# Kernel tuning notes

Hardware: AMD Instinct MI355X
Metric: run time of the kernel (lower is better)

Reference implementation:

```python
import jax, jax.numpy as jnp
import numpy as np

B, C, H, W = 8, 512, 32, 32
NUM_HEADS, D_K = 8, 64
EPS = 1e-5


def setup_inputs() -> dict:
    key = jax.random.key(0)
    ks = jax.random.split(key, 6)
    s = 1.0 / np.sqrt(C)
    return {
        "x": jax.random.normal(ks[0], (B, C, H, W), dtype=jnp.float32),
        "wq": jax.random.uniform(ks[1], (C, NUM_HEADS * D_K), jnp.float32, -s, s),
        "bq": jnp.zeros((NUM_HEADS * D_K,), jnp.float32),
        "wk": jax.random.uniform(ks[2], (C, NUM_HEADS * D_K), jnp.float32, -s, s),
        "bk": jnp.zeros((NUM_HEADS * D_K,), jnp.float32),
        "wv": jax.random.uniform(ks[3], (C, NUM_HEADS * D_K), jnp.float32, -s, s),
        "bv": jnp.zeros((NUM_HEADS * D_K,), jnp.float32),
        "ln_g": jnp.ones((C,), jnp.float32),
        "ln_b": jnp.zeros((C,), jnp.float32),
        "wo": jax.random.uniform(ks[4], (NUM_HEADS * D_K, C), jnp.float32, -s, s),
        "bo": jnp.zeros((C,), jnp.float32),
    }


def reference(x, wq, bq, wk, bk, wv, bv, ln_g, ln_b, wo, bo):
    b, c, h, w = x.shape
    seq = h * w
    # [B, C, H, W] -> [B, S, C]
    t = x.reshape(b, c, seq).transpose(0, 2, 1)
    residual = t
    # LayerNorm over channel dim
    mu = jnp.mean(t, axis=-1, keepdims=True)
    var = jnp.var(t, axis=-1, keepdims=True)
    tn = (t - mu) * jax.lax.rsqrt(var + EPS) * ln_g + ln_b
    # QKV projections -> [B, S, h, d]
    q = (tn @ wq + bq).reshape(b, seq, NUM_HEADS, D_K)
    k = (tn @ wk + bk).reshape(b, seq, NUM_HEADS, D_K)
    v = (tn @ wv + bv).reshape(b, seq, NUM_HEADS, D_K)
    scores = jnp.einsum("bqhd,bkhd->bhqk", q, k) / np.sqrt(D_K).astype(np.float32)
    attn = jax.nn.softmax(scores, axis=-1)
    out = jnp.einsum("bhqk,bkhd->bqhd", attn, v).reshape(b, seq, NUM_HEADS * D_K)
    out = out @ wo + bo
    return out + residual
```

## Files before the change

kernel.cpp:

```cpp
#include <hip/hip_runtime.h>
#include <hip/hip_bf16.h>
#include <stdint.h>

#define BB 8
#define CC 512
#define SS 1024
#define NH 8
#define DK 64
#define MM (BB*SS)
#define PQ 72
#define LNP 40

typedef __attribute__((ext_vector_type(8))) short bf16x8;
typedef __attribute__((ext_vector_type(4))) float f32x4;

__device__ inline float b2f(unsigned short u) {
    union { unsigned int i; float f; } x; x.i = ((unsigned int)u) << 16; return x.f;
}
__device__ inline unsigned short f2b(float f) {
    union { float f; unsigned int i; } x; x.f = f;
    unsigned int r = (x.i + 0x7FFFu + ((x.i >> 16) & 1u)) >> 16;
    return (unsigned short)r;
}
__device__ inline unsigned int cvtpk(float lo, float hi) {
    unsigned int r;
    asm("v_cvt_pk_bf16_f32 %0, %1, %2" : "=v"(r) : "v"(lo), "v"(hi));
    return r;
}
__device__ inline f32x4 mfma16(bf16x8 a, bf16x8 b, f32x4 c) {
    return __builtin_amdgcn_mfma_f32_16x16x32_bf16(a, b, c, 0, 0, 0);
}
__device__ __forceinline__ void gload16(const void* g, void* l) {
    __builtin_amdgcn_global_load_lds(
        (const __attribute__((address_space(1))) void*)g,
        (__attribute__((address_space(3))) void*)l, 16, 0, 0);
}

__global__ void __launch_bounds__(256) wtrans_kernel(const float* __restrict__ wq,
                                                     const float* __restrict__ wk,
                                                     const float* __restrict__ wv,
                                                     const float* __restrict__ wo,
                                                     unsigned short* __restrict__ wT) {
    __shared__ float lds[64][65];
    const float* w = (blockIdx.z == 0) ? wq : (blockIdx.z == 1) ? wk : (blockIdx.z == 2) ? wv : wo;
    unsigned short* o = wT + (size_t)blockIdx.z * (512 * 512);
    const int n0 = blockIdx.x * 64, k0 = blockIdx.y * 64;
    const int t = threadIdx.x;
    {
        const int nl = (t & 15) * 4, kr = t >> 4;
#pragma unroll
        for (int i = 0; i < 4; ++i) {
            float4 v = *(const float4*)(w + (size_t)(k0 + kr + i * 16) * 512 + n0 + nl);
            lds[kr + i * 16][nl] = v.x; lds[kr + i * 16][nl + 1] = v.y;
            lds[kr + i * 16][nl + 2] = v.z; lds[kr + i * 16][nl + 3] = v.w;
        }
    }
    __syncthreads();
    {
        const int k8 = (t & 7) * 8, nr = t >> 3;
#pragma unroll
        for (int ii = 0; ii < 2; ++ii) {
            int n = nr + ii * 32;
            unsigned short pk[8];
#pragma unroll
            for (int e = 0; e < 8; ++e) pk[e] = f2b(lds[k8 + e][n]);
            *(uint4*)&o[(size_t)(n0 + n) * 512 + k0 + k8] = *(uint4*)pk;
        }
    }
}

__global__ void __launch_bounds__(256) xlnf_kernel(const float* __restrict__ x,
                                                   const float* __restrict__ g,
                                                   const float* __restrict__ bta,
                                                   unsigned short* __restrict__ xt,
                                                   unsigned short* __restrict__ tn) {
    __shared__ unsigned short raw[512 * LNP];
    __shared__ float2 red[32][33];
    __shared__ float2 stf[32];
    const int b = blockIdx.y, s0 = blockIdx.x * 32;
    const int t = threadIdx.x;
    const int sl4 = (t & 7) * 4, crow = t >> 3;
    float sum[4] = {0.f, 0.f, 0.f, 0.f}, sq[4] = {0.f, 0.f, 0.f, 0.f};
#pragma unroll
    for (int ci = 0; ci < 16; ++ci) {
        const int c = crow + 32 * ci;
        float4 v = *(const float4*)(x + ((size_t)b * 512 + c) * 1024 + s0 + sl4);
        sum[0] += v.x; sq[0] += v.x * v.x;
        sum[1] += v.y; sq[1] += v.y * v.y;
        sum[2] += v.z; sq[2] += v.z * v.z;
        sum[3] += v.w; sq[3] += v.w * v.w;
        const int swz = ((c >> 6) & 3) << 3;
        uint2 pk;
        pk.x = (unsigned int)f2b(v.x) | ((unsigned int)f2b(v.y) << 16);
        pk.y = (unsigned int)f2b(v.z) | ((unsigned int)f2b(v.w) << 16);
        *(uint2*)&raw[c * LNP + (sl4 ^ swz)] = pk;
    }
#pragma unroll
    for (int e = 0; e < 4; ++e) red[crow][sl4 + e] = make_float2(sum[e], sq[e]);
    __syncthreads();
    if (t < 32) {
        float s = 0.f, q = 0.f;
#pragma unroll
        for (int cg = 0; cg < 32; ++cg) { s += red[cg][t].x; q += red[cg][t].y; }
        float mean = s * (1.f / 512.f);
        float var = q * (1.f / 512.f) - mean * mean;
        stf[t] = make_float2(mean, rsqrtf(var + 1e-5f));
    }
    __syncthreads();
    {
        const int srow = t >> 3, cb = (t & 7) * 64;
        const float2 st = stf[srow];
        const size_t orow = ((size_t)b * 1024 + s0 + srow) * 512;
#pragma unroll
        for (int cc = 0; cc < 64; cc += 8) {
            const int c0 = cb + cc;
            unsigned short rv[8], nv[8];
            const float4 g0 = *(const float4*)(g + c0), g1 = *(const float4*)(g + c0 + 4);
            const float4 b0 = *(const float4*)(bta + c0), b1 = *(const float4*)(bta + c0 + 4);
            const float gg[8] = {g0.x, g0.y, g0.z, g0.w, g1.x, g1.y, g1.z, g1.w};
            const float bb[8] = {b0.x, b0.y, b0.z, b0.w, b1.x, b1.y, b1.z, b1.w};
#pragma unroll
            for (int e = 0; e < 8; ++e) {
                const int c = c0 + e;
                const int swz = ((c >> 6) & 3) << 3;
                unsigned short u = raw[c * LNP + (srow ^ swz)];
                rv[e] = u;
                nv[e] = f2b((b2f(u) - st.x) * st.y * gg[e] + bb[e]);
            }
            *(uint4*)&xt[orow + c0] = *(uint4*)rv;
            *(uint4*)&tn[orow + c0] = *(uint4*)nv;
        }
    }
}

template <bool SWAP>
__device__ inline void gemm_tile(const unsigned short* __restrict__ A,
                                 const unsigned short* __restrict__ Bt,
                                 int m0, int n0,
                                 unsigned short (*A_lds)[128 * 64],
                                 unsigned short (*B_lds)[128 * 64],
                                 f32x4 acc[4][4]) {
    const int t = threadIdx.x;
    const int lane = t & 63, w = t >> 6;
    const int l15 = lane & 15, l4 = lane >> 4;
    const int wm = (w >> 1) * 64, wn = (w & 1) * 64;
    auto STAGE = [&](int bi, int kt) {
#pragma unroll
        for (int i = 0; i < 4; ++i) {
            int chunk = i * 256 + t;
            int row = chunk >> 3, kc = (chunk & 7) * 8;
            gload16(A + (size_t)(m0 + row) * 512 + kt * 64 + kc, &A_lds[bi][chunk * 8]);
            gload16(Bt + (size_t)(n0 + row) * 512 + kt * 64 + kc, &B_lds[bi][chunk * 8]);
        }
    };
    STAGE(0, 0);
    __syncthreads();
#pragma unroll 1
    for (int kt = 0; kt < 8; ++kt) {
        const int bi = kt & 1;
        if (kt < 7) STAGE(bi ^ 1, kt + 1);
#pragma unroll
        for (int kk = 0; kk < 2; ++kk) {
            bf16x8 af[4], bfr[4];
#pragma unroll
            for (int i = 0; i < 4; ++i)
                af[i] = *(const bf16x8*)&A_lds[bi][(wm + i * 16 + l15) * 64 + kk * 32 + l4 * 8];
#pragma unroll
            for (int j = 0; j < 4; ++j)
                bfr[j] = *(const bf16x8*)&B_lds[bi][(wn + j * 16 + l15) * 64 + kk * 32 + l4 * 8];
#pragma unroll
            for (int i = 0; i < 4; ++i)
#pragma unroll
                for (int j = 0; j < 4; ++j)
                    acc[i][j] = SWAP ? mfma16(bfr[j], af[i], acc[i][j])
                                     : mfma16(af[i], bfr[j], acc[i][j]);
        }
        __syncthreads();
    }
}

__global__ void __launch_bounds__(256) gemm_qkv_kernel(const unsigned short* __restrict__ tn,
                                                       const unsigned short* __restrict__ wT,
                                                       const float* __restrict__ bq,
                                                       const float* __restrict__ bk,
                                                       const float* __restrict__ bv,
                                                       unsigned short* __restrict__ outbase) {
    __shared__ alignas(16) unsigned short A_lds[2][128 * 64];
    __shared__ alignas(16) unsigned short B_lds[2][128 * 64];
    const int z = blockIdx.z;
    const unsigned short* Bt = wT + (size_t)z * (512 * 512);
    const float* bias = (z == 0) ? bq : (z == 1) ? bk : bv;
    const int m0 = blockIdx.x * 128, n0 = blockIdx.y * 128;
    f32x4 acc[4][4];
    const f32x4 z4 = {0.f, 0.f, 0.f, 0.f};
#pragma unroll
    for (int i = 0; i < 4; ++i)
#pragma unroll
        for (int j = 0; j < 4; ++j) acc[i][j] = z4;
    const int lane = threadIdx.x & 63, w = threadIdx.x >> 6;
    const int l15 = lane & 15, l4 = lane >> 4;
    const int wm = (w >> 1) * 64, wn = (w & 1) * 64;
    if (z < 2) {
        gemm_tile<true>(tn, Bt, m0, n0, A_lds, B_lds, acc);
        unsigned short* out = outbase + (size_t)z * MM * 512;
        float4 bias4[4];
#pragma unroll
        for (int j = 0; j < 4; ++j)
            bias4[j] = *(const float4*)(bias + n0 + wn + j * 16 + l4 * 4);
#pragma unroll
        for (int i = 0; i < 4; ++i) {
            const size_t row = (size_t)(m0 + wm + i * 16 + l15);
#pragma unroll
            for (int j = 0; j < 4; ++j) {
                const int nc = n0 + wn + j * 16 + l4 * 4;
                uint2 pk;
                pk.x = (unsigned int)f2b(acc[i][j][0] + bias4[j].x) |
                       ((unsigned int)f2b(acc[i][j][1] + bias4[j].y) << 16);
                pk.y = (unsigned int)f2b(acc[i][j][2] + bias4[j].z) |
                       ((unsigned int)f2b(acc[i][j][3] + bias4[j].w) << 16);
                *(uint2*)&out[row * 512 + nc] = pk;
            }
        }
    } else {
        gemm_tile<false>(tn, Bt, m0, n0, A_lds, B_lds, acc);
        unsigned short* vt = outbase + (size_t)2 * MM * 512;
#pragma unroll
        for (int i = 0; i < 4; ++i)
#pragma unroll
            for (int j = 0; j < 4; ++j) {
                int col = n0 + wn + j * 16 + l15;
                float bcol = bias[col];
                int rowb = m0 + wm + i * 16 + l4 * 4;
                int bi = rowb >> 10, s0 = rowb & 1023;
                uint2 pk;
                pk.x = (unsigned int)f2b(acc[i][j][0] + bcol) |
                       ((unsigned int)f2b(acc[i][j][1] + bcol) << 16);
                pk.y = (unsigned int)f2b(acc[i][j][2] + bcol) |
                       ((unsigned int)f2b(acc[i][j][3] + bcol) << 16);
                *(uint2*)&vt[((size_t)bi * 512 + col) * 1024 + s0] = pk;
            }
    }
}

__global__ void __launch_bounds__(512) attn_kernel(const unsigned short* __restrict__ q,
                                                   const unsigned short* __restrict__ k,
                                                   const unsigned short* __restrict__ vt,
                                                   unsigned short* __restrict__ o) {
    __shared__ alignas(16) unsigned short Kl[2][64 * 64];
    __shared__ alignas(16) unsigned short Vl[2][64 * 64];
    __shared__ alignas(16) unsigned short Pl[8][16 * PQ];
    const int pid = blockIdx.x;
    const int g = (pid >> 6) * 8 + (pid & 7);
    const int qt = (pid >> 3) & 7;
    const int b = g >> 3, h = g & 7;
    const int t = threadIdx.x, lane = t & 63, w = t >> 6;
    const int l15 = lane & 15, l4 = lane >> 4;

    const float QSC = 0.125f * 1.44269504f;
    const int qrow = qt * 128 + w * 16 + l15;
    const unsigned short* qp = q + ((size_t)(b * SS + qrow)) * 512 + h * 64;
    bf16x8 qf[2];
#pragma unroll
    for (int kk = 0; kk < 2; ++kk) {
        bf16x8 tmp = *(const bf16x8*)(qp + kk * 32 + l4 * 8);
#pragma unroll
        for (int e = 0; e < 8; ++e)
            tmp[e] = (short)f2b(b2f((unsigned short)tmp[e]) * QSC);
        qf[kk] = tmp;
    }

    const int srow = t >> 3;
    const int scb = ((t & 7) * 16) ^ ((srow & 7) << 4);
    const char* kptr = (const char*)(k + ((size_t)(b * SS) + srow) * 512 + h * 64) + scb;
    const char* vptr = (const char*)(vt + ((size_t)(b * NH + h) * DK + srow) * SS) + scb;

    float m_run = -1e30f, l_run = 0.f;
    f32x4 acc_o[4];
    const f32x4 z4 = {0.f, 0.f, 0.f, 0.f};
#pragma unroll
    for (int j = 0; j < 4; ++j) acc_o[j] = z4;

    gload16(kptr, &Kl[0][t * 8]);
    gload16(vptr, &Vl[0][t * 8]);
    kptr += 64 * 512 * 2;
    vptr += 64 * 2;
    __syncthreads();

#pragma unroll 1
    for (int kt = 0; kt < 16; ++kt) {
        const int bi = kt & 1;
        if (kt < 15) {
            gload16(kptr, &Kl[bi ^ 1][t * 8]);
            gload16(vptr, &Vl[bi ^ 1][t * 8]);
            kptr += 64 * 512 * 2;
            vptr += 64 * 2;
        }

        f32x4 sc[4];
#pragma unroll
        for (int j = 0; j < 4; ++j) sc[j] = z4;
#pragma unroll
        for (int kk = 0; kk < 2; ++kk)
#pragma unroll
            for (int j = 0; j < 4; ++j) {
                int row = j * 16 + l15;
                int cb = (kk * 64 + l4 * 16) ^ ((row & 7) << 4);
                bf16x8 kf = *(const bf16x8*)((const char*)Kl[bi] + row * 128 + cb);
                sc[j] = mfma16(kf, qf[kk], sc[j]);
            }

        float mx = fmaxf(fmaxf(sc[0][0], sc[0][1]), fmaxf(sc[0][2], sc[0][3]));
#pragma unroll
        for (int j = 1; j < 4; ++j)
            mx = fmaxf(mx, fmaxf(fmaxf(sc[j][0], sc[j][1]), fmaxf(sc[j][2], sc[j][3])));
        mx = fmaxf(mx, __shfl_xor(mx, 16));
        mx = fmaxf(mx, __shfl_xor(mx, 32));
        const float mnew = fmaxf(m_run, mx);
        const float scl = exp2f(m_run - mnew);
        m_run = mnew;

        float p[4][4], lsum = 0.f;
#pragma unroll
        for (int j = 0; j < 4; ++j)
#pragma unroll
            for (int r = 0; r < 4; ++r) {
                p[j][r] = exp2f(sc[j][r] - mnew);
                lsum += p[j][r];
            }
        l_run = l_run * scl + lsum;

#pragma unroll
        for (int j = 0; j < 4; ++j) {
            uint2 pk;
            pk.x = cvtpk(p[j][0], p[j][1]);
            pk.y = cvtpk(p[j][2], p[j][3]);
            *(uint2*)&Pl[w][l15 * PQ + j * 16 + l4 * 4] = pk;
        }

        float scl_r[4];
#pragma unroll
        for (int r = 0; r < 4; ++r) scl_r[r] = __shfl(scl, (l4 << 2) | r);
#pragma unroll
        for (int j = 0; j < 4; ++j)
#pragma unroll
            for (int r = 0; r < 4; ++r) acc_o[j][r] *= scl_r[r];

#pragma unroll
        for (int kk = 0; kk < 2; ++kk) {
            bf16x8 pf = *(const bf16x8*)&Pl[w][l15 * PQ + kk * 32 + l4 * 8];
#pragma unroll
            for (int j = 0; j < 4; ++j) {
                int row = j * 16 + l15;
                int cb = (kk * 64 + l4 * 16) ^ ((row & 7) << 4);
                bf16x8 vf = *(const bf16x8*)((const char*)Vl[bi] + row * 128 + cb);
                acc_o[j] = mfma16(pf, vf, acc_o[j]);
            }
        }

        __syncthreads();
    }

    float l_tot = l_run;
    l_tot += __shfl_xor(l_tot, 16);
    l_tot += __shfl_xor(l_tot, 32);
    float l_r[4];
#pragma unroll
    for (int r = 0; r < 4; ++r) l_r[r] = __shfl(l_tot, (l4 << 2) | r);

#pragma unroll
    for (int j = 0; j < 4; ++j)
#pragma unroll
        for (int r = 0; r < 4; ++r) {
            int row = qt * 128 + w * 16 + l4 * 4 + r;
            float val = acc_o[j][r] / l_r[r];
            o[((size_t)(b * SS + row)) * 512 + h * 64 + j * 16 + l15] = f2b(val);
        }
}

__global__ void __launch_bounds__(256) gemm_out_kernel(const unsigned short* __restrict__ ao,
                                                       const unsigned short* __restrict__ woT,
                                                       const float* __restrict__ bo,
                                                       const unsigned short* __restrict__ xt,
                                                       float* __restrict__ out) {
    __shared__ alignas(16) unsigned short A_lds[2][128 * 64];
    __shared__ alignas(16) unsigned short B_lds[2][128 * 64];
    const int m0 = blockIdx.x * 128, n0 = blockIdx.y * 128;
    f32x4 acc[4][4];
    const f32x4 z4 = {0.f, 0.f, 0.f, 0.f};
#pragma unroll
    for (int i = 0; i < 4; ++i)
#pragma unroll
        for (int j = 0; j < 4; ++j) acc[i][j] = z4;
    gemm_tile<true>(ao, woT, m0, n0, A_lds, B_lds, acc);
    const int lane = threadIdx.x & 63, w = threadIdx.x >> 6;
    const int l15 = lane & 15, l4 = lane >> 4;
    const int wm = (w >> 1) * 64, wn = (w & 1) * 64;
    float4 bias4[4];
#pragma unroll
    for (int j = 0; j < 4; ++j)
        bias4[j] = *(const float4*)(bo + n0 + wn + j * 16 + l4 * 4);
#pragma unroll
    for (int i = 0; i < 4; ++i) {
        const size_t row = (size_t)(m0 + wm + i * 16 + l15);
#pragma unroll
        for (int j = 0; j < 4; ++j) {
            const int nc = n0 + wn + j * 16 + l4 * 4;
            uint2 rv = *(const uint2*)&xt[row * 512 + nc];
            float4 o4;
            o4.x = acc[i][j][0] + bias4[j].x + b2f((unsigned short)(rv.x & 0xffff));
            o4.y = acc[i][j][1] + bias4[j].y + b2f((unsigned short)(rv.x >> 16));
            o4.z = acc[i][j][2] + bias4[j].z + b2f((unsigned short)(rv.y & 0xffff));
            o4.w = acc[i][j][3] + bias4[j].w + b2f((unsigned short)(rv.y >> 16));
            *(float4*)&out[row * 512 + nc] = o4;
        }
    }
}

extern "C" void kernel_launch(void* const* d_in, const int* in_sizes, int n_in,
                              void* d_out, int out_size, void* d_ws, size_t ws_size,
                              hipStream_t stream) {
    const float* x   = (const float*)d_in[0];
    const float* wq  = (const float*)d_in[1];
    const float* bq  = (const float*)d_in[2];
    const float* wk  = (const float*)d_in[3];
    const float* bk  = (const float*)d_in[4];
    const float* wv  = (const float*)d_in[5];
    const float* bv  = (const float*)d_in[6];
    const float* lng = (const float*)d_in[7];
    const float* lnb = (const float*)d_in[8];
    const float* wo  = (const float*)d_in[9];
    const float* bo  = (const float*)d_in[10];
    float* out = (float*)d_out;

    unsigned short* ws  = (unsigned short*)d_ws;
    const size_t M1 = (size_t)1024 * 1024;
    unsigned short* tn   = ws;
    unsigned short* qkvb = ws + 4 * M1;
    unsigned short* wT   = ws + 16 * M1;
    unsigned short* xt   = ws + 17 * M1;
    unsigned short* ao   = tn;

    wtrans_kernel<<<dim3(8, 8, 4), 256, 0, stream>>>(wq, wk, wv, wo, wT);
    xlnf_kernel<<<dim3(32, 8), 256, 0, stream>>>(x, lng, lnb, xt, tn);
    gemm_qkv_kernel<<<dim3(64, 4, 3), 256, 0, stream>>>(tn, wT, bq, bk, bv, qkvb);
    attn_kernel<<<512, 512, 0, stream>>>(qkvb,
                                         qkvb + (size_t)MM * 512,
                                         qkvb + (size_t)2 * MM * 512,
                                         ao);
    gemm_out_kernel<<<dim3(64, 4), 256, 0, stream>>>(ao, wT + (size_t)3 * 512 * 512, bo, xt, out);
}
```

Measured before the change: 181.4 us.

## Merge prep kernels, fuse QKV GEMMs sharing A tile, swizzle LDS layout

Combines the weight transpose and the LayerNorm kernels into one launch that dispatches on block index. Rewrites the QKV GEMM so each block loads one 128-row A tile and computes Q, K and V for a 64-column slice, so the activation tile is reused across three weights instead of being loaded three times. Adds an XOR swizzle to the LDS layout of the GEMM tiles to reduce bank conflicts on fragment reads. The trade-off is fewer blocks per GEMM launch, higher register pressure from 24 accumulators, and larger shared memory in the prep kernel.

```diff
diff --git a/kernel.cpp b/kernel.cpp
--- a/kernel.cpp
+++ b/kernel.cpp
@@ -36,99 +36,102 @@
         (__attribute__((address_space(3))) void*)l, 16, 0, 0);
 }
 
-__global__ void __launch_bounds__(256) wtrans_kernel(const float* __restrict__ wq,
-                                                     const float* __restrict__ wk,
-                                                     const float* __restrict__ wv,
-                                                     const float* __restrict__ wo,
-                                                     unsigned short* __restrict__ wT) {
-    __shared__ float lds[64][65];
-    const float* w = (blockIdx.z == 0) ? wq : (blockIdx.z == 1) ? wk : (blockIdx.z == 2) ? wv : wo;
-    unsigned short* o = wT + (size_t)blockIdx.z * (512 * 512);
-    const int n0 = blockIdx.x * 64, k0 = blockIdx.y * 64;
-    const int t = threadIdx.x;
-    {
-        const int nl = (t & 15) * 4, kr = t >> 4;
-#pragma unroll
-        for (int i = 0; i < 4; ++i) {
-            float4 v = *(const float4*)(w + (size_t)(k0 + kr + i * 16) * 512 + n0 + nl);
-            lds[kr + i * 16][nl] = v.x; lds[kr + i * 16][nl + 1] = v.y;
-            lds[kr + i * 16][nl + 2] = v.z; lds[kr + i * 16][nl + 3] = v.w;
-        }
-    }
-    __syncthreads();
-    {
-        const int k8 = (t & 7) * 8, nr = t >> 3;
-#pragma unroll
-        for (int ii = 0; ii < 2; ++ii) {
-            int n = nr + ii * 32;
-            unsigned short pk[8];
-#pragma unroll
-            for (int e = 0; e < 8; ++e) pk[e] = f2b(lds[k8 + e][n]);
-            *(uint4*)&o[(size_t)(n0 + n) * 512 + k0 + k8] = *(uint4*)pk;
-        }
-    }
-}
-
-__global__ void __launch_bounds__(256) xlnf_kernel(const float* __restrict__ x,
+__global__ void __launch_bounds__(256) prep_kernel(const float* __restrict__ wq,
+                                                   const float* __restrict__ wk,
+                                                   const float* __restrict__ wv,
+                                                   const float* __restrict__ wo,
+                                                   unsigned short* __restrict__ wT,
+                                                   const float* __restrict__ x,
                                                    const float* __restrict__ g,
                                                    const float* __restrict__ bta,
                                                    unsigned short* __restrict__ xt,
                                                    unsigned short* __restrict__ tn) {
-    __shared__ unsigned short raw[512 * LNP];
-    __shared__ float2 red[32][33];
-    __shared__ float2 stf[32];
-    const int b = blockIdx.y, s0 = blockIdx.x * 32;
+    __shared__ alignas(16) char smem[49664];
     const int t = threadIdx.x;
-    const int sl4 = (t & 7) * 4, crow = t >> 3;
-    float sum[4] = {0.f, 0.f, 0.f, 0.f}, sq[4] = {0.f, 0.f, 0.f, 0.f};
-#pragma unroll
-    for (int ci = 0; ci < 16; ++ci) {
-        const int c = crow + 32 * ci;
-        float4 v = *(const float4*)(x + ((size_t)b * 512 + c) * 1024 + s0 + sl4);
-        sum[0] += v.x; sq[0] += v.x * v.x;
-        sum[1] += v.y; sq[1] += v.y * v.y;
-        sum[2] += v.z; sq[2] += v.z * v.z;
-        sum[3] += v.w; sq[3] += v.w * v.w;
-        const int swz = ((c >> 6) & 3) << 3;
-        uint2 pk;
-        pk.x = (unsigned int)f2b(v.x) | ((unsigned int)f2b(v.y) << 16);
-        pk.y = (unsigned int)f2b(v.z) | ((unsigned int)f2b(v.w) << 16);
-        *(uint2*)&raw[c * LNP + (sl4 ^ swz)] = pk;
-    }
-#pragma unroll
-    for (int e = 0; e < 4; ++e) red[crow][sl4 + e] = make_float2(sum[e], sq[e]);
-    __syncthreads();
-    if (t < 32) {
-        float s = 0.f, q = 0.f;
-#pragma unroll
-        for (int cg = 0; cg < 32; ++cg) { s += red[cg][t].x; q += red[cg][t].y; }
-        float mean = s * (1.f / 512.f);
-        float var = q * (1.f / 512.f) - mean * mean;
-        stf[t] = make_float2(mean, rsqrtf(var + 1e-5f));
-    }
-    __syncthreads();
-    {
-        const int srow = t >> 3, cb = (t & 7) * 64;
-        const float2 st = stf[srow];
-        const size_t orow = ((size_t)b * 1024 + s0 + srow) * 512;
-#pragma unroll
-        for (int cc = 0; cc < 64; cc += 8) {
-            const int c0 = cb + cc;
-            unsigned short rv[8], nv[8];
-            const float4 g0 = *(const float4*)(g + c0), g1 = *(const float4*)(g + c0 + 4);
-            const float4 b0 = *(const float4*)(bta + c0), b1 = *(const float4*)(bta + c0 + 4);
-            const float gg[8] = {g0.x, g0.y, g0.z, g0.w, g1.x, g1.y, g1.z, g1.w};
-            const float bb[8] = {b0.x, b0.y, b0.z, b0.w, b1.x, b1.y, b1.z, b1.w};
-#pragma unroll
-            for (int e = 0; e < 8; ++e) {
-                const int c = c0 + e;
-                const int swz = ((c >> 6) & 3) << 3;
-                unsigned short u = raw[c * LNP + (srow ^ swz)];
-                rv[e] = u;
-                nv[e] = f2b((b2f(u) - st.x) * st.y * gg[e] + bb[e]);
-            }
-            *(uint4*)&xt[orow + c0] = *(uint4*)rv;
-            *(uint4*)&tn[orow + c0] = *(uint4*)nv;
+    if (blockIdx.x < 256) {
+        float (*lds)[65] = (float(*)[65])smem;
+        const int bz = blockIdx.x >> 6, bx = (blockIdx.x >> 3) & 7, by = blockIdx.x & 7;
+        const float* w = (bz == 0) ? wq : (bz == 1) ? wk : (bz == 2) ? wv : wo;
+        unsigned short* o = wT + (size_t)bz * (512 * 512);
+        const int n0 = bx * 64, k0 = by * 64;
+        {
+            const int nl = (t & 15) * 4, kr = t >> 4;
+#pragma unroll
+            for (int i = 0; i < 4; ++i) {
+                float4 v = *(const float4*)(w + (size_t)(k0 + kr + i * 16) * 512 + n0 + nl);
+                lds[kr + i * 16][nl] = v.x; lds[kr + i * 16][nl + 1] = v.y;
+                lds[kr + i * 16][nl + 2] = v.z; lds[kr + i * 16][nl + 3] = v.w;
+            }
+        }
+        __syncthreads();
+        {
+            const int k8 = (t & 7) * 8, nr = t >> 3;
+#pragma unroll
+            for (int ii = 0; ii < 2; ++ii) {
+                int n = nr + ii * 32;
+                unsigned short pk[8];
+#pragma unroll
+                for (int e = 0; e < 8; ++e) pk[e] = f2b(lds[k8 + e][n]);
+                *(uint4*)&o[(size_t)(n0 + n) * 512 + k0 + k8] = *(uint4*)pk;
+            }
+        }
+    } else {
+        unsigned short* raw = (unsigned short*)smem;
+        float2 (*red)[33] = (float2(*)[33])(smem + 40960);
+        float2* stf = (float2*)(smem + 49408);
+        const int idx = blockIdx.x - 256;
+        const int b = idx >> 5, s0 = (idx & 31) * 32;
+        const int sl4 = (t & 7) * 4, crow = t >> 3;
+        float sum[4] = {0.f, 0.f, 0.f, 0.f}, sq[4] = {0.f, 0.f, 0.f, 0.f};
+#pragma unroll
+        for (int ci = 0; ci < 16; ++ci) {
+            const int c = crow + 32 * ci;
+            float4 v = *(const float4*)(x + ((size_t)b * 512 + c) * 1024 + s0 + sl4);
+            sum[0] += v.x; sq[0] += v.x * v.x;
+            sum[1] += v.y; sq[1] += v.y * v.y;
+            sum[2] += v.z; sq[2] += v.z * v.z;
+            sum[3] += v.w; sq[3] += v.w * v.w;
+            const int swz = ((c >> 6) & 3) << 3;
+            uint2 pk;
+            pk.x = (unsigned int)f2b(v.x) | ((unsigned int)f2b(v.y) << 16);
+            pk.y = (unsigned int)f2b(v.z) | ((unsigned int)f2b(v.w) << 16);
+            *(uint2*)&raw[c * LNP + (sl4 ^ swz)] = pk;
+        }
+#pragma unroll
+        for (int e = 0; e < 4; ++e) red[crow][sl4 + e] = make_float2(sum[e], sq[e]);
+        __syncthreads();
+        if (t < 32) {
+            float s = 0.f, q = 0.f;
+#pragma unroll
+            for (int cg = 0; cg < 32; ++cg) { s += red[cg][t].x; q += red[cg][t].y; }
+            float mean = s * (1.f / 512.f);
+            float var = q * (1.f / 512.f) - mean * mean;
+            stf[t] = make_float2(mean, rsqrtf(var + 1e-5f));
+        }
+        __syncthreads();
+        {
+            const int srow = t >> 3, cb = (t & 7) * 64;
+            const float2 st = stf[srow];
+            const size_t orow = ((size_t)b * 1024 + s0 + srow) * 512;
+#pragma unroll
+            for (int cc = 0; cc < 64; cc += 8) {
+                const int c0 = cb + cc;
+                unsigned short rv[8], nv[8];
+                const float4 g0 = *(const float4*)(g + c0), g1 = *(const float4*)(g + c0 + 4);
+                const float4 b0 = *(const float4*)(bta + c0), b1 = *(const float4*)(bta + c0 + 4);
+                const float gg[8] = {g0.x, g0.y, g0.z, g0.w, g1.x, g1.y, g1.z, g1.w};
+                const float bb[8] = {b0.x, b0.y, b0.z, b0.w, b1.x, b1.y, b1.z, b1.w};
+#pragma unroll
+                for (int e = 0; e < 8; ++e) {
+                    const int c = c0 + e;
+                    const int swz = ((c >> 6) & 3) << 3;
+                    unsigned short u = raw[c * LNP + (srow ^ swz)];
+                    rv[e] = u;
+                    nv[e] = f2b((b2f(u) - st.x) * st.y * gg[e] + bb[e]);
+                }
+                *(uint4*)&xt[orow + c0] = *(uint4*)rv;
+                *(uint4*)&tn[orow + c0] = *(uint4*)nv;
+            }
         }
     }
 }
@@ -148,9 +151,12 @@
 #pragma unroll
         for (int i = 0; i < 4; ++i) {
             int chunk = i * 256 + t;
-            int row = chunk >> 3, kc = (chunk & 7) * 8;
-            gload16(A + (size_t)(m0 + row) * 512 + kt * 64 + kc, &A_lds[bi][chunk * 8]);
-            gload16(Bt + (size_t)(n0 + row) * 512 + kt * 64 + kc, &B_lds[bi][chunk * 8]);
+            int row = chunk >> 3;
+            int sb = ((chunk & 7) * 16) ^ ((row & 7) << 4);
+            gload16((const char*)(A + (size_t)(m0 + row) * 512 + kt * 64) + sb,
+                    &A_lds[bi][chunk * 8]);
+            gload16((const char*)(Bt + (size_t)(n0 + row) * 512 + kt * 64) + sb,
+                    &B_lds[bi][chunk * 8]);
         }
     };
     STAGE(0, 0);
@@ -163,11 +169,17 @@
         for (int kk = 0; kk < 2; ++kk) {
             bf16x8 af[4], bfr[4];
 #pragma unroll
-            for (int i = 0; i < 4; ++i)
-                af[i] = *(const bf16x8*)&A_lds[bi][(wm + i * 16 + l15) * 64 + kk * 32 + l4 * 8];
-#pragma unroll
-            for (int j = 0; j < 4; ++j)
-                bfr[j] = *(const bf16x8*)&B_lds[bi][(wn + j * 16 + l15) * 64 + kk * 32 + l4 * 8];
+            for (int i = 0; i < 4; ++i) {
+                int row = wm + i * 16 + l15;
+                int cb = (kk * 64 + l4 * 16) ^ ((row & 7) << 4);
+                af[i] = *(const bf16x8*)((const char*)A_lds[bi] + row * 128 + cb);
+            }
+#pragma unroll
+            for (int j = 0; j < 4; ++j) {
+                int row = wn + j * 16 + l15;
+                int cb = (kk * 64 + l4 * 16) ^ ((row & 7) << 4);
+                bfr[j] = *(const bf16x8*)((const char*)B_lds[bi] + row * 128 + cb);
+            }
 #pragma unroll
             for (int i = 0; i < 4; ++i)
 #pragma unroll
@@ -179,65 +191,121 @@
     }
 }
 
-__global__ void __launch_bounds__(256) gemm_qkv_kernel(const unsigned short* __restrict__ tn,
-                                                       const unsigned short* __restrict__ wT,
-                                                       const float* __restrict__ bq,
-                                                       const float* __restrict__ bk,
-                                                       const float* __restrict__ bv,
-                                                       unsigned short* __restrict__ outbase) {
+__global__ void __launch_bounds__(256) gemm_qkvf_kernel(const unsigned short* __restrict__ tn,
+                                                        const unsigned short* __restrict__ wT,
+                                                        const float* __restrict__ bq,
+                                                        const float* __restrict__ bk,
+                                                        const float* __restrict__ bv,
+                                                        unsigned short* __restrict__ outbase) {
     __shared__ alignas(16) unsigned short A_lds[2][128 * 64];
-    __shared__ alignas(16) unsigned short B_lds[2][128 * 64];
-    const int z = blockIdx.z;
-    const unsigned short* Bt = wT + (size_t)z * (512 * 512);
-    const float* bias = (z == 0) ? bq : (z == 1) ? bk : bv;
-    const int m0 = blockIdx.x * 128, n0 = blockIdx.y * 128;
-    f32x4 acc[4][4];
+    __shared__ alignas(16) unsigned short B_lds[2][3][64 * 64];
+    const int m0 = blockIdx.x * 128, n0 = blockIdx.y * 64;
+    const int t = threadIdx.x, lane = t & 63, w = t >> 6;
+    const int l15 = lane & 15, l4 = lane >> 4;
+    const int wm = w * 32;
+    f32x4 acc[3][2][4];
     const f32x4 z4 = {0.f, 0.f, 0.f, 0.f};
 #pragma unroll
-    for (int i = 0; i < 4; ++i)
-#pragma unroll
-        for (int j = 0; j < 4; ++j) acc[i][j] = z4;
-    const int lane = threadIdx.x & 63, w = threadIdx.x >> 6;
-    const int l15 = lane & 15, l4 = lane >> 4;
-    const int wm = (w >> 1) * 64, wn = (w & 1) * 64;
-    if (z < 2) {
-        gemm_tile<true>(tn, Bt, m0, n0, A_lds, B_lds, acc);
+    for (int z = 0; z < 3; ++z)
+#pragma unroll
+        for (int i = 0; i < 2; ++i)
+#pragma unroll
+            for (int j = 0; j < 4; ++j) acc[z][i][j] = z4;
+
+    auto STAGE = [&](int bi, int kt) {
+#pragma unroll
+        for (int i = 0; i < 4; ++i) {
+            int chunk = i * 256 + t;
+            int row = chunk >> 3;
+            int sb = ((chunk & 7) * 16) ^ ((row & 7) << 4);
+            gload16((const char*)(tn + (size_t)(m0 + row) * 512 + kt * 64) + sb,
+                    &A_lds[bi][chunk * 8]);
+        }
+#pragma unroll
+        for (int z = 0; z < 3; ++z)
+#pragma unroll
+            for (int i = 0; i < 2; ++i) {
+                int chunk = i * 256 + t;
+                int row = chunk >> 3;
+                int sb = ((chunk & 7) * 16) ^ ((row & 7) << 4);
+                gload16((const char*)(wT + (size_t)z * 512 * 512 +
+                                      (size_t)(n0 + row) * 512 + kt * 64) + sb,
+                        &B_lds[bi][z][chunk * 8]);
+            }
+    };
+    STAGE(0, 0);
+    __syncthreads();
+#pragma unroll 1
+    for (int kt = 0; kt < 8; ++kt) {
+        const int bi = kt & 1;
+        if (kt < 7) STAGE(bi ^ 1, kt + 1);
+#pragma unroll
+        for (int kk = 0; kk < 2; ++kk) {
+            bf16x8 af[2];
+#pragma unroll
+            for (int i = 0; i < 2; ++i) {
+                int row = wm + i * 16 + l15;
+                int cb = (kk * 64 + l4 * 16) ^ ((row & 7) << 4);
+                af[i] = *(const bf16x8*)((const char*)A_lds[bi] + row * 128 + cb);
+            }
+#pragma unroll
+            for (int z = 0; z < 3; ++z) {
+                bf16x8 bfr[4];
+#pragma unroll
+                for (int j = 0; j < 4; ++j) {
+                    int row = j * 16 + l15;
+                    int cb = (kk * 64 + l4 * 16) ^ ((row & 7) << 4);
+                    bfr[j] = *(const bf16x8*)((const char*)B_lds[bi][z] + row * 128 + cb);
+                }
+#pragma unroll
+                for (int i = 0; i < 2; ++i)
+#pragma unroll
+                    for (int j = 0; j < 4; ++j)
+                        acc[z][i][j] = (z < 2) ? mfma16(bfr[j], af[i], acc[z][i][j])
+                                               : mfma16(af[i], bfr[j], acc[z][i][j]);
+            }
+        }
+        __syncthreads();
+    }
+#pragma unroll
+    for (int z = 0; z < 2; ++z) {
+        const float* bias = (z == 0) ? bq : bk;
         unsigned short* out = outbase + (size_t)z * MM * 512;
         float4 bias4[4];
 #pragma unroll
         for (int j = 0; j < 4; ++j)
-            bias4[j] = *(const float4*)(bias + n0 + wn + j * 16 + l4 * 4);
-#pragma unroll
-        for (int i = 0; i < 4; ++i) {
+            bias4[j] = *(const float4*)(bias + n0 + j * 16 + l4 * 4);
+#pragma unroll
+        for (int i = 0; i < 2; ++i) {
             const size_t row = (size_t)(m0 + wm + i * 16 + l15);
 #pragma unroll
             for (int j = 0; j < 4; ++j) {
-                const int nc = n0 + wn + j * 16 + l4 * 4;
+                const int nc = n0 + j * 16 + l4 * 4;
                 uint2 pk;
-                pk.x = (unsigned int)f2b(acc[i][j][0] + bias4[j].x) |
-                       ((unsigned int)f2b(acc[i][j][1] + bias4[j].y) << 16);
-                pk.y = (unsigned int)f2b(acc[i][j][2] + bias4[j].z) |
-                       ((unsigned int)f2b(acc[i][j][3] + bias4[j].w) << 16);
+                pk.x = (unsigned int)f2b(acc[z][i][j][0] + bias4[j].x) |
+                       ((unsigned int)f2b(acc[z][i][j][1] + bias4[j].y) << 16);
+                pk.y = (unsigned int)f2b(acc[z][i][j][2] + bias4[j].z) |
+                       ((unsigned int)f2b(acc[z][i][j][3] + bias4[j].w) << 16);
                 *(uint2*)&out[row * 512 + nc] = pk;
             }
         }
-    } else {
-        gemm_tile<false>(tn, Bt, m0, n0, A_lds, B_lds, acc);
+    }
+    {
         unsigned short* vt = outbase + (size_t)2 * MM * 512;
 #pragma unroll
-        for (int i = 0; i < 4; ++i)
+        for (int i = 0; i < 2; ++i)
 #pragma unroll
             for (int j = 0; j < 4; ++j) {
-                int col = n0 + wn + j * 16 + l15;
-                float bcol = bias[col];
+                int col = n0 + j * 16 + l15;
+                float bcol = bv[col];
                 int rowb = m0 + wm + i * 16 + l4 * 4;
-                int bi = rowb >> 10, s0 = rowb & 1023;
+                int bi_ = rowb >> 10, s0 = rowb & 1023;
                 uint2 pk;
-                pk.x = (unsigned int)f2b(acc[i][j][0] + bcol) |
-                       ((unsigned int)f2b(acc[i][j][1] + bcol) << 16);
-                pk.y = (unsigned int)f2b(acc[i][j][2] + bcol) |
-                       ((unsigned int)f2b(acc[i][j][3] + bcol) << 16);
-                *(uint2*)&vt[((size_t)bi * 512 + col) * 1024 + s0] = pk;
+                pk.x = (unsigned int)f2b(acc[2][i][j][0] + bcol) |
+                       ((unsigned int)f2b(acc[2][i][j][1] + bcol) << 16);
+                pk.y = (unsigned int)f2b(acc[2][i][j][2] + bcol) |
+                       ((unsigned int)f2b(acc[2][i][j][3] + bcol) << 16);
+                *(uint2*)&vt[((size_t)bi_ * 512 + col) * 1024 + s0] = pk;
             }
     }
 }
@@ -440,9 +508,8 @@
     unsigned short* xt   = ws + 17 * M1;
     unsigned short* ao   = tn;
 
-    wtrans_kernel<<<dim3(8, 8, 4), 256, 0, stream>>>(wq, wk, wv, wo, wT);
-    xlnf_kernel<<<dim3(32, 8), 256, 0, stream>>>(x, lng, lnb, xt, tn);
-    gemm_qkv_kernel<<<dim3(64, 4, 3), 256, 0, stream>>>(tn, wT, bq, bk, bv, qkvb);
+    prep_kernel<<<512, 256, 0, stream>>>(wq, wk, wv, wo, wT, x, lng, lnb, xt, tn);
+    gemm_qkvf_kernel<<<dim3(64, 8), 256, 0, stream>>>(tn, wT, bq, bk, bv, qkvb);
     attn_kernel<<<512, 512, 0, stream>>>(qkvb,
                                          qkvb + (size_t)MM * 512,
                                          qkvb + (size_t)2 * MM * 512,
```

Measured after the change: 169.1 us. 6.8% less time.
